# Performance work log

Measured on AMD Instinct MI355X. Metric: run time of the kernel, lower is better.

## Reference

```python
import jax, jax.numpy as jnp
import numpy as np

N_ATOMS = 100000
N_RES = 12500
N_EDGES = 800000
D = 115
D_IN = 37
N_LAYERS = 4


def _sage_conv(x, src, dst, Wl_i, Wr_i, bl_i):
    """PyG SAGEConv (aggr='mean', root_weight=True): lin_l(mean_j x_j) + lin_r(x)."""
    n = x.shape[0]
    deg = jax.ops.segment_sum(jnp.ones(src.shape[0], x.dtype), dst, num_segments=n)
    agg = jax.ops.segment_sum(x[src], dst, num_segments=n)  # [N, D] gather+scatter
    agg = agg / jnp.maximum(deg, 1.0)[:, None]
    return agg @ Wl_i.T + bl_i + x @ Wr_i.T


def setup_inputs() -> dict:
    key = jax.random.key(0)
    ks = jax.random.split(key, 8)
    resid_embedding = jax.random.normal(ks[0], (N_RES, D), dtype=jnp.float32)
    atom_onehot_embedding = jax.random.normal(ks[1], (N_ATOMS, D_IN), dtype=jnp.float32)
    edge_index_atom = jax.random.randint(ks[2], (2, N_EDGES), 0, N_ATOMS, dtype=jnp.int32)
    res2atom_map = jnp.sort(jax.random.randint(ks[3], (N_ATOMS,), 0, N_RES, dtype=jnp.int32))
    ln_W = jax.random.normal(ks[4], (D, D_IN), dtype=jnp.float32) / np.sqrt(D_IN)
    ln_b = jnp.zeros((D,), dtype=jnp.float32)
    Wl = jax.random.normal(ks[5], (N_LAYERS, D, D), dtype=jnp.float32) / np.sqrt(D)
    Wr = jax.random.normal(ks[6], (N_LAYERS, D, D), dtype=jnp.float32) / np.sqrt(D)
    bl = jnp.zeros((N_LAYERS, D), dtype=jnp.float32)
    return {
        "resid_embedding": resid_embedding,
        "atom_onehot_embedding": atom_onehot_embedding,
        "edge_index_atom": edge_index_atom,
        "res2atom_map": res2atom_map,
        "ln_W": ln_W,
        "ln_b": ln_b,
        "Wl": Wl,
        "Wr": Wr,
        "bl": bl,
    }


def reference(resid_embedding, atom_onehot_embedding, edge_index_atom, res2atom_map,
              ln_W, ln_b, Wl, Wr, bl):
    src, dst = edge_index_atom[0], edge_index_atom[1]
    # input projection: Linear(37 -> 115)
    x = atom_onehot_embedding @ ln_W.T + ln_b
    # four chained SAGEConv layers (no activation between them, per source)
    for i in range(N_LAYERS):
        x = _sage_conv(x, src, dst, Wl[i], Wr[i], bl[i])
    # atom2residue: scatter-sum pooling of atom features into residues
    n_res = resid_embedding.shape[0]
    feats_atom = jax.ops.segment_sum(x, res2atom_map, num_segments=n_res)  # [N_RES, D]
    return feats_atom
```

## Files before the change

kernel.cpp:

```cpp
#include <hip/hip_runtime.h>
#include <hip/hip_bf16.h>

#define N_ATOMS 100000
#define N_RES   12500
#define N_EDGES 800000
#define D_IN    37
#define D       115
#define DP      128
#define MPAD    100096
#define N_LAYERS 4
#define SCE     1024
#define NSCB    ((N_ATOMS + SCE - 1) / SCE)
#define KPROJ   64
#define LSTRIDE 72

typedef __bf16 bf16x8 __attribute__((ext_vector_type(8)));
typedef float  f32x4  __attribute__((ext_vector_type(4)));
typedef unsigned int u32x4 __attribute__((ext_vector_type(4)));

__device__ __forceinline__ unsigned short f2bf(float f) {
  unsigned u = __builtin_bit_cast(unsigned, f);
  u += 0x7fffu + ((u >> 16) & 1u);
  return (unsigned short)(u >> 16);
}
__device__ __forceinline__ float bf2f(unsigned short h) {
  unsigned u = ((unsigned)h) << 16;
  return __builtin_bit_cast(float, u);
}
__device__ __forceinline__ bf16x8 ld_frag(const unsigned short* p) {
  u32x4 u = *reinterpret_cast<const u32x4*>(p);
  return __builtin_bit_cast(bf16x8, u);
}

__global__ void k_hist_edges(const int* __restrict__ eidx, int* __restrict__ hist) {
  int e = blockIdx.x * blockDim.x + threadIdx.x;
  if (e < N_EDGES) atomicAdd(&hist[eidx[N_EDGES + e]], 1);
}

__global__ __launch_bounds__(256) void k_scan_part(
    const int* __restrict__ cnt, int* __restrict__ bsum)
{
  __shared__ int sh[256];
  const int t = threadIdx.x, b = blockIdx.x;
  const int base = b * SCE + t * 4;
  int s = 0;
  #pragma unroll
  for (int i = 0; i < 4; ++i) { int id = base + i; if (id < N_ATOMS) s += cnt[id]; }
  sh[t] = s; __syncthreads();
  for (int d = 128; d > 0; d >>= 1) { if (t < d) sh[t] += sh[t + d]; __syncthreads(); }
  if (t == 0) bsum[b] = sh[0];
}
__global__ __launch_bounds__(256) void k_scan_bsum(
    int* __restrict__ bsum, int* __restrict__ total)
{
  __shared__ int sh[256];
  const int t = threadIdx.x;
  int v = (t < NSCB) ? bsum[t] : 0;
  sh[t] = v; __syncthreads();
  for (int d = 1; d < 256; d <<= 1) {
    int u = (t >= d) ? sh[t - d] : 0;
    __syncthreads();
    sh[t] += u;
    __syncthreads();
  }
  if (t < NSCB) bsum[t] = sh[t] - v;
  if (t == 255) *total = sh[255];
}
__global__ __launch_bounds__(256) void k_scan_final(
    const int* __restrict__ cnt, const int* __restrict__ bsum,
    int* __restrict__ offs, int* __restrict__ cursor, float* __restrict__ invdeg)
{
  __shared__ int sh[256];
  const int t = threadIdx.x, b = blockIdx.x;
  const int base = b * SCE + t * 4;
  int c[4]; int s = 0;
  #pragma unroll
  for (int i = 0; i < 4; ++i) {
    int id = base + i;
    c[i] = (id < N_ATOMS) ? cnt[id] : 0;
    s += c[i];
  }
  sh[t] = s; __syncthreads();
  for (int d = 1; d < 256; d <<= 1) {
    int u = (t >= d) ? sh[t - d] : 0;
    __syncthreads();
    sh[t] += u;
    __syncthreads();
  }
  int run = bsum[b] + sh[t] - s;
  #pragma unroll
  for (int i = 0; i < 4; ++i) {
    int id = base + i;
    if (id < N_ATOMS) {
      offs[id] = run;
      cursor[id] = run;
      invdeg[id] = 1.0f / (float)max(c[i], 1);
      run += c[i];
    }
  }
}

__global__ __launch_bounds__(256) void k_res_bounds(
    const int* __restrict__ r2a, int* __restrict__ res_start)
{
  int r = blockIdx.x * blockDim.x + threadIdx.x;
  if (r > N_RES) return;
  int lo = 0, hi = N_ATOMS;
  while (lo < hi) {
    int mid = (lo + hi) >> 1;
    if (r2a[mid] < r) lo = mid + 1; else hi = mid;
  }
  res_start[r] = lo;
}

__global__ void k_fill(const int* __restrict__ eidx, int* __restrict__ cursor,
                       int* __restrict__ srcs) {
  int e = blockIdx.x * blockDim.x + threadIdx.x;
  if (e < N_EDGES) {
    int s = eidx[e], d = eidx[N_EDGES + e];
    int pos = atomicAdd(&cursor[d], 1);
    srcs[pos] = s;
  }
}

__global__ void k_convw(const float* __restrict__ Wl, const float* __restrict__ Wr,
                        unsigned short* __restrict__ wpad)
{
  const int k = threadIdx.x;
  const int c = blockIdx.x;
  const int m = blockIdx.y;
  const float* src = (m < 4) ? (Wl + m * D * D) : (Wr + (m - 4) * D * D);
  unsigned short v = 0;
  if (c < D && k < D) v = f2bf(src[c * D + k]);
  wpad[(m * 128 + c) * 128 + k] = v;
}

__global__ __launch_bounds__(256) void k_proj(
    const float* __restrict__ A, const float* __restrict__ Wf,
    const float* __restrict__ bf, unsigned short* __restrict__ xout)
{
  __shared__ unsigned short sA[128 * LSTRIDE];
  __shared__ unsigned short sW[128 * LSTRIDE];
  const int t = threadIdx.x;
  const int r0 = blockIdx.x * 128;

  for (int idx = t; idx < 128 * KPROJ; idx += 256) {
    const int row = idx >> 6, k = idx & 63;
    const int gr = r0 + row;
    unsigned short v = 0;
    if (k < D_IN && gr < N_ATOMS) v = f2bf(A[(size_t)gr * D_IN + k]);
    sA[row * LSTRIDE + k] = v;
  }
  for (int idx = t; idx < 128 * KPROJ; idx += 256) {
    const int col = idx >> 6, k = idx & 63;
    unsigned short v = 0;
    if (col < D && k < D_IN) v = f2bf(Wf[col * D_IN + k]);
    sW[col * LSTRIDE + k] = v;
  }
  __syncthreads();

  const int lane = t & 63;
  const int wid  = t >> 6;
  const int wrow = wid * 32;
  const int lrow = lane & 15;
  const int koff = (lane >> 4) * 8;

  f32x4 acc[2][8];
  #pragma unroll
  for (int i = 0; i < 2; ++i)
    #pragma unroll
    for (int j = 0; j < 8; ++j)
      acc[i][j] = (f32x4){0.f, 0.f, 0.f, 0.f};

  #pragma unroll
  for (int ks = 0; ks < 2; ++ks) {
    const int k0 = ks * 32 + koff;
    bf16x8 a0 = ld_frag(&sA[(wrow + lrow) * LSTRIDE + k0]);
    bf16x8 a1 = ld_frag(&sA[(wrow + 16 + lrow) * LSTRIDE + k0]);
    #pragma unroll
    for (int ct = 0; ct < 8; ++ct) {
      bf16x8 b = ld_frag(&sW[(ct * 16 + lrow) * LSTRIDE + k0]);
      acc[0][ct] = __builtin_amdgcn_mfma_f32_16x16x32_bf16(a0, b, acc[0][ct], 0, 0, 0);
      acc[1][ct] = __builtin_amdgcn_mfma_f32_16x16x32_bf16(a1, b, acc[1][ct], 0, 0, 0);
    }
  }

  const int ocol = lane & 15;
  const int orow = (lane >> 4) * 4;
  #pragma unroll
  for (int ct = 0; ct < 8; ++ct) {
    const int col = ct * 16 + ocol;
    const float bv = (col < D) ? bf[col] : 0.f;
    #pragma unroll
    for (int rt = 0; rt < 2; ++rt) {
      #pragma unroll
      for (int j = 0; j < 4; ++j) {
        const int grow = r0 + wrow + rt * 16 + orow + j;
        if (grow < N_ATOMS)
          xout[(size_t)grow * DP + col] = f2bf(acc[rt][ct][j] + bv);
      }
    }
  }
}

__global__ __launch_bounds__(256) void k_agg(
    const unsigned int* __restrict__ xin, const int* __restrict__ row_start,
    const int* __restrict__ srcs, const float* __restrict__ invdeg,
    unsigned int* __restrict__ aggout)
{
  const int w = (int)((blockIdx.x * 256 + threadIdx.x) >> 6);
  const int lane = threadIdx.x & 63;
  if (w >= N_ATOMS) return;
  const int beg = row_start[w], end = row_start[w + 1];
  float a0 = 0.f, a1 = 0.f;
  for (int base = beg; base < end; base += 16) {
    const int m = end - base;
    int sidx = 0;
    if (lane < 16 && lane < m) sidx = srcs[base + lane];
    #pragma unroll
    for (int j = 0; j < 16; ++j) {
      const int s = __shfl(sidx, j);
      const unsigned int v = xin[(size_t)s * 64 + lane];
      if (j < m) {
        a0 += bf2f((unsigned short)(v & 0xffffu));
        a1 += bf2f((unsigned short)(v >> 16));
      }
    }
  }
  const float sc = invdeg[w];
  unsigned int o = (unsigned int)f2bf(a0 * sc) | ((unsigned int)f2bf(a1 * sc) << 16);
  aggout[w * 64 + lane] = o;
}

__global__ __launch_bounds__(256) void k_gemm(
    const unsigned short* __restrict__ agg,
    const unsigned short* __restrict__ xin,
    const unsigned short* __restrict__ wl,
    const unsigned short* __restrict__ wr,
    const float* __restrict__ bias,
    unsigned short* __restrict__ xout)
{
  const int lane = threadIdx.x & 63;
  const int wid  = threadIdx.x >> 6;
  const int row0 = blockIdx.x * 128 + wid * 32;
  const int lrow = lane & 15;
  const int koff = (lane >> 4) * 8;

  f32x4 acc[2][8];
  #pragma unroll
  for (int i = 0; i < 2; ++i)
    #pragma unroll
    for (int j = 0; j < 8; ++j)
      acc[i][j] = (f32x4){0.f, 0.f, 0.f, 0.f};

  #pragma unroll
  for (int s = 0; s < 2; ++s) {
    const unsigned short* X = s ? xin : agg;
    const unsigned short* W = s ? wr : wl;
    #pragma unroll
    for (int ks = 0; ks < 4; ++ks) {
      const int k0 = ks * 32 + koff;
      bf16x8 a0 = ld_frag(&X[(size_t)(row0 + lrow) * DP + k0]);
      bf16x8 a1 = ld_frag(&X[(size_t)(row0 + 16 + lrow) * DP + k0]);
      #pragma unroll
      for (int ct = 0; ct < 8; ++ct) {
        bf16x8 b = ld_frag(&W[(ct * 16 + lrow) * DP + k0]);
        acc[0][ct] = __builtin_amdgcn_mfma_f32_16x16x32_bf16(a0, b, acc[0][ct], 0, 0, 0);
        acc[1][ct] = __builtin_amdgcn_mfma_f32_16x16x32_bf16(a1, b, acc[1][ct], 0, 0, 0);
      }
    }
  }

  const int ocol = lane & 15;
  const int orow = (lane >> 4) * 4;
  #pragma unroll
  for (int ct = 0; ct < 8; ++ct) {
    const int col = ct * 16 + ocol;
    const float bv = (col < D) ? bias[col] : 0.f;
    #pragma unroll
    for (int rt = 0; rt < 2; ++rt) {
      #pragma unroll
      for (int j = 0; j < 4; ++j) {
        const int grow = row0 + rt * 16 + orow + j;
        if (grow < N_ATOMS)
          xout[(size_t)grow * DP + col] = f2bf(acc[rt][ct][j] + bv);
      }
    }
  }
}

__global__ __launch_bounds__(256) void k_pool(
    const unsigned int* __restrict__ x, const int* __restrict__ res_start,
    float* __restrict__ out)
{
  const int r = (int)((blockIdx.x * 256 + threadIdx.x) >> 6);
  const int lane = threadIdx.x & 63;
  if (r >= N_RES) return;
  const int beg = res_start[r], end = res_start[r + 1];
  float a0 = 0.f, a1 = 0.f;
  for (int a = beg; a < end; ++a) {
    unsigned int v = x[a * 64 + lane];
    a0 += bf2f((unsigned short)(v & 0xffffu));
    a1 += bf2f((unsigned short)(v >> 16));
  }
  const int c0 = lane * 2;
  if (c0 < D)     out[(size_t)r * D + c0]     = a0;
  if (c0 + 1 < D) out[(size_t)r * D + c0 + 1] = a1;
}

extern "C" void kernel_launch(void* const* d_in, const int* in_sizes, int n_in,
                              void* d_out, int out_size, void* d_ws, size_t ws_size,
                              hipStream_t stream)
{
  (void)in_sizes; (void)n_in; (void)out_size; (void)ws_size;
  const float* atom_emb = (const float*)d_in[1];
  const int*   eidx     = (const int*)d_in[2];
  const int*   r2a      = (const int*)d_in[3];
  const float* lnW      = (const float*)d_in[4];
  const float* lnb      = (const float*)d_in[5];
  const float* Wl       = (const float*)d_in[6];
  const float* Wr       = (const float*)d_in[7];
  const float* bl       = (const float*)d_in[8];
  float* out = (float*)d_out;

  char* p = (char*)d_ws;
  auto alloc = [&](size_t b) { char* r = p; p += (b + 255) & ~(size_t)255; return r; };
  unsigned short* xb0  = (unsigned short*)alloc((size_t)MPAD * DP * 2);
  unsigned short* xb1  = (unsigned short*)alloc((size_t)MPAD * DP * 2);
  unsigned short* xb2  = (unsigned short*)alloc((size_t)MPAD * DP * 2);
  unsigned short* wpad = (unsigned short*)alloc((size_t)8 * 128 * 128 * 2);
  int*   hist      = (int*)alloc((size_t)N_ATOMS * 4);
  int*   row_start = (int*)alloc((size_t)(N_ATOMS + 1) * 4);
  int*   cursor    = (int*)alloc((size_t)N_ATOMS * 4);
  float* invdeg    = (float*)alloc((size_t)N_ATOMS * 4);
  int*   srcs      = (int*)alloc((size_t)N_EDGES * 4);
  int*   bsum      = (int*)alloc((size_t)256 * 4);
  int*   res_start = (int*)alloc((size_t)(N_RES + 1) * 4);

  hipMemsetAsync(hist, 0, (size_t)N_ATOMS * 4, stream);

  k_convw<<<dim3(128, 8), 128, 0, stream>>>(Wl, Wr, wpad);
  k_hist_edges<<<(N_EDGES + 255) / 256, 256, 0, stream>>>(eidx, hist);
  k_scan_part<<<NSCB, 256, 0, stream>>>(hist, bsum);
  k_scan_bsum<<<1, 256, 0, stream>>>(bsum, row_start + N_ATOMS);
  k_scan_final<<<NSCB, 256, 0, stream>>>(hist, bsum, row_start, cursor, invdeg);
  k_res_bounds<<<(N_RES + 1 + 255) / 256, 256, 0, stream>>>(r2a, res_start);
  k_fill<<<(N_EDGES + 255) / 256, 256, 0, stream>>>(eidx, cursor, srcs);
  k_proj<<<MPAD / 128, 256, 0, stream>>>(atom_emb, lnW, lnb, xb0);

  unsigned short* bufs[3] = {xb0, xb1, xb2};
  int cur = 0;
  for (int l = 0; l < N_LAYERS; ++l) {
    unsigned short* xin  = bufs[cur];
    unsigned short* aggb = bufs[(cur + 1) % 3];
    unsigned short* xo   = bufs[(cur + 2) % 3];
    k_agg<<<(N_ATOMS * 64) / 256, 256, 0, stream>>>(
        (const unsigned int*)xin, row_start, srcs, invdeg, (unsigned int*)aggb);
    k_gemm<<<MPAD / 128, 256, 0, stream>>>(
        aggb, xin, wpad + (size_t)l * 16384, wpad + (size_t)(4 + l) * 16384,
        bl + (size_t)l * D, xo);
    cur = (cur + 2) % 3;
  }
  k_pool<<<(N_RES * 64) / 256, 256, 0, stream>>>(
      (const unsigned int*)bufs[cur], res_start, out);
}
```

Before: 732.6 us.

## Fuse neighbor mean aggregation into per-layer GEMM via LDS tile

Merges the separate aggregation and GEMM kernels into one per-layer kernel. Each 128-row block first gathers neighbor features, with 16 threads per row each loading 16-byte chunks, and writes the scaled mean into a padded LDS tile. It then runs the MFMA GEMM from LDS for the aggregated term and from global memory for the root term. This removes the global write and re-read of the aggregated buffer and one launch per layer. The cost is less parallelism in the gather (one block per 128 rows, 782 blocks), sequential per-row loops within each thread group, and higher LDS usage that may reduce occupancy.

```diff
diff --git a/kernel.cpp b/kernel.cpp
--- a/kernel.cpp
+++ b/kernel.cpp
@@ -13,6 +13,7 @@
 #define NSCB    ((N_ATOMS + SCE - 1) / SCE)
 #define KPROJ   64
 #define LSTRIDE 72
+#define LSTR2   136
 
 typedef __bf16 bf16x8 __attribute__((ext_vector_type(8)));
 typedef float  f32x4  __attribute__((ext_vector_type(4)));
@@ -203,46 +204,59 @@
   }
 }
 
-__global__ __launch_bounds__(256) void k_agg(
-    const unsigned int* __restrict__ xin, const int* __restrict__ row_start,
-    const int* __restrict__ srcs, const float* __restrict__ invdeg,
-    unsigned int* __restrict__ aggout)
-{
-  const int w = (int)((blockIdx.x * 256 + threadIdx.x) >> 6);
-  const int lane = threadIdx.x & 63;
-  if (w >= N_ATOMS) return;
-  const int beg = row_start[w], end = row_start[w + 1];
-  float a0 = 0.f, a1 = 0.f;
-  for (int base = beg; base < end; base += 16) {
-    const int m = end - base;
-    int sidx = 0;
-    if (lane < 16 && lane < m) sidx = srcs[base + lane];
-    #pragma unroll
-    for (int j = 0; j < 16; ++j) {
-      const int s = __shfl(sidx, j);
-      const unsigned int v = xin[(size_t)s * 64 + lane];
-      if (j < m) {
-        a0 += bf2f((unsigned short)(v & 0xffffu));
-        a1 += bf2f((unsigned short)(v >> 16));
-      }
-    }
-  }
-  const float sc = invdeg[w];
-  unsigned int o = (unsigned int)f2bf(a0 * sc) | ((unsigned int)f2bf(a1 * sc) << 16);
-  aggout[w * 64 + lane] = o;
-}
-
-__global__ __launch_bounds__(256) void k_gemm(
-    const unsigned short* __restrict__ agg,
+__global__ __launch_bounds__(256) void k_layer(
     const unsigned short* __restrict__ xin,
+    const int* __restrict__ row_start,
+    const int* __restrict__ srcs,
+    const float* __restrict__ invdeg,
     const unsigned short* __restrict__ wl,
     const unsigned short* __restrict__ wr,
     const float* __restrict__ bias,
     unsigned short* __restrict__ xout)
 {
-  const int lane = threadIdx.x & 63;
-  const int wid  = threadIdx.x >> 6;
-  const int row0 = blockIdx.x * 128 + wid * 32;
+  __shared__ unsigned short sAgg[128 * LSTR2];
+  const int t = threadIdx.x;
+  const int r0 = blockIdx.x * 128;
+  const int rp = t >> 4;
+  const int ql = t & 15;
+
+  for (int i = 0; i < 8; ++i) {
+    const int row = rp * 8 + i;
+    const int grow = r0 + row;
+    float a[8] = {0.f,0.f,0.f,0.f,0.f,0.f,0.f,0.f};
+    float sc = 0.f;
+    if (grow < N_ATOMS) {
+      const int beg = row_start[grow], end = row_start[grow + 1];
+      sc = invdeg[grow];
+      for (int b2 = beg; b2 < end; b2 += 16) {
+        const int m = end - b2;
+        int sidx = 0;
+        if (ql < m) sidx = srcs[b2 + ql];
+        #pragma unroll
+        for (int j = 0; j < 16; ++j) {
+          if (j < m) {
+            const int s = __shfl(sidx, (t & 48) + j);
+            const u32x4 v = *(reinterpret_cast<const u32x4*>(xin + (size_t)s * DP) + ql);
+            #pragma unroll
+            for (int q = 0; q < 4; ++q) {
+              a[2*q]   += bf2f((unsigned short)(v[q] & 0xffffu));
+              a[2*q+1] += bf2f((unsigned short)(v[q] >> 16));
+            }
+          }
+        }
+      }
+    }
+    unsigned int w[4];
+    #pragma unroll
+    for (int q = 0; q < 4; ++q)
+      w[q] = (unsigned int)f2bf(a[2*q] * sc) | ((unsigned int)f2bf(a[2*q+1] * sc) << 16);
+    *reinterpret_cast<u32x4*>(&sAgg[row * LSTR2 + ql * 8]) = (u32x4){w[0], w[1], w[2], w[3]};
+  }
+  __syncthreads();
+
+  const int lane = t & 63;
+  const int wid  = t >> 6;
+  const int wrow = wid * 32;
   const int lrow = lane & 15;
   const int koff = (lane >> 4) * 8;
 
@@ -254,20 +268,27 @@
       acc[i][j] = (f32x4){0.f, 0.f, 0.f, 0.f};
 
   #pragma unroll
-  for (int s = 0; s < 2; ++s) {
-    const unsigned short* X = s ? xin : agg;
-    const unsigned short* W = s ? wr : wl;
-    #pragma unroll
-    for (int ks = 0; ks < 4; ++ks) {
-      const int k0 = ks * 32 + koff;
-      bf16x8 a0 = ld_frag(&X[(size_t)(row0 + lrow) * DP + k0]);
-      bf16x8 a1 = ld_frag(&X[(size_t)(row0 + 16 + lrow) * DP + k0]);
-      #pragma unroll
-      for (int ct = 0; ct < 8; ++ct) {
-        bf16x8 b = ld_frag(&W[(ct * 16 + lrow) * DP + k0]);
-        acc[0][ct] = __builtin_amdgcn_mfma_f32_16x16x32_bf16(a0, b, acc[0][ct], 0, 0, 0);
-        acc[1][ct] = __builtin_amdgcn_mfma_f32_16x16x32_bf16(a1, b, acc[1][ct], 0, 0, 0);
-      }
+  for (int ks = 0; ks < 4; ++ks) {
+    const int k0 = ks * 32 + koff;
+    bf16x8 a0 = ld_frag(&sAgg[(wrow + lrow) * LSTR2 + k0]);
+    bf16x8 a1 = ld_frag(&sAgg[(wrow + 16 + lrow) * LSTR2 + k0]);
+    #pragma unroll
+    for (int ct = 0; ct < 8; ++ct) {
+      bf16x8 b = ld_frag(&wl[(ct * 16 + lrow) * DP + k0]);
+      acc[0][ct] = __builtin_amdgcn_mfma_f32_16x16x32_bf16(a0, b, acc[0][ct], 0, 0, 0);
+      acc[1][ct] = __builtin_amdgcn_mfma_f32_16x16x32_bf16(a1, b, acc[1][ct], 0, 0, 0);
+    }
+  }
+  #pragma unroll
+  for (int ks = 0; ks < 4; ++ks) {
+    const int k0 = ks * 32 + koff;
+    bf16x8 a0 = ld_frag(&xin[(size_t)(r0 + wrow + lrow) * DP + k0]);
+    bf16x8 a1 = ld_frag(&xin[(size_t)(r0 + wrow + 16 + lrow) * DP + k0]);
+    #pragma unroll
+    for (int ct = 0; ct < 8; ++ct) {
+      bf16x8 b = ld_frag(&wr[(ct * 16 + lrow) * DP + k0]);
+      acc[0][ct] = __builtin_amdgcn_mfma_f32_16x16x32_bf16(a0, b, acc[0][ct], 0, 0, 0);
+      acc[1][ct] = __builtin_amdgcn_mfma_f32_16x16x32_bf16(a1, b, acc[1][ct], 0, 0, 0);
     }
   }
 
@@ -281,7 +302,7 @@
     for (int rt = 0; rt < 2; ++rt) {
       #pragma unroll
       for (int j = 0; j < 4; ++j) {
-        const int grow = row0 + rt * 16 + orow + j;
+        const int grow = r0 + wrow + rt * 16 + orow + j;
         if (grow < N_ATOMS)
           xout[(size_t)grow * DP + col] = f2bf(acc[rt][ct][j] + bv);
       }
@@ -327,7 +348,6 @@
   auto alloc = [&](size_t b) { char* r = p; p += (b + 255) & ~(size_t)255; return r; };
   unsigned short* xb0  = (unsigned short*)alloc((size_t)MPAD * DP * 2);
   unsigned short* xb1  = (unsigned short*)alloc((size_t)MPAD * DP * 2);
-  unsigned short* xb2  = (unsigned short*)alloc((size_t)MPAD * DP * 2);
   unsigned short* wpad = (unsigned short*)alloc((size_t)8 * 128 * 128 * 2);
   int*   hist      = (int*)alloc((size_t)N_ATOMS * 4);
   int*   row_start = (int*)alloc((size_t)(N_ATOMS + 1) * 4);
@@ -348,19 +368,15 @@
   k_fill<<<(N_EDGES + 255) / 256, 256, 0, stream>>>(eidx, cursor, srcs);
   k_proj<<<MPAD / 128, 256, 0, stream>>>(atom_emb, lnW, lnb, xb0);
 
-  unsigned short* bufs[3] = {xb0, xb1, xb2};
-  int cur = 0;
+  unsigned short* cur = xb0;
+  unsigned short* nxt = xb1;
   for (int l = 0; l < N_LAYERS; ++l) {
-    unsigned short* xin  = bufs[cur];
-    unsigned short* aggb = bufs[(cur + 1) % 3];
-    unsigned short* xo   = bufs[(cur + 2) % 3];
-    k_agg<<<(N_ATOMS * 64) / 256, 256, 0, stream>>>(
-        (const unsigned int*)xin, row_start, srcs, invdeg, (unsigned int*)aggb);
-    k_gemm<<<MPAD / 128, 256, 0, stream>>>(
-        aggb, xin, wpad + (size_t)l * 16384, wpad + (size_t)(4 + l) * 16384,
-        bl + (size_t)l * D, xo);
-    cur = (cur + 2) % 3;
+    k_layer<<<MPAD / 128, 256, 0, stream>>>(
+        cur, row_start, srcs, invdeg,
+        wpad + (size_t)l * 16384, wpad + (size_t)(4 + l) * 16384,
+        bl + (size_t)l * D, nxt);
+    unsigned short* tmp = cur; cur = nxt; nxt = tmp;
   }
   k_pool<<<(N_RES * 64) / 256, 256, 0, stream>>>(
-      (const unsigned int*)bufs[cur], res_start, out);
-}
+      (const unsigned int*)cur, res_start, out);
+}
```

After: 788.5 us. 7.6% more time.

## Exploit layer linearity: propagate raw features, pool per hop, fold weights

Applied to the files above, without the earlier changes.

There is no activation between the SAGE layers, so the whole network is linear. The per-layer MFMA GEMMs are replaced by repeated mean-aggregation of the projected features. Each hop's result is pooled into residues, and a small weight-polynomial matrix per hop is built from Wl, Wr and the biases, with a ones column carrying the bias. A final fp32 kernel combines the five pooled stacks with these matrices. This removes four full-size atom GEMMs and their global traffic. In exchange it adds extra pooling passes, tiny serial matrix-product launches and a scalar, non-MFMA final contraction, and it changes where rounding happens.

```diff
diff --git a/kernel.cpp b/kernel.cpp
--- a/kernel.cpp
+++ b/kernel.cpp
@@ -123,16 +123,60 @@
   }
 }
 
-__global__ void k_convw(const float* __restrict__ Wl, const float* __restrict__ Wr,
-                        unsigned short* __restrict__ wpad)
-{
-  const int k = threadIdx.x;
-  const int c = blockIdx.x;
-  const int m = blockIdx.y;
-  const float* src = (m < 4) ? (Wl + m * D * D) : (Wr + (m - 4) * D * D);
-  unsigned short v = 0;
-  if (c < D && k < D) v = f2bf(src[c * D + k]);
-  wpad[(m * 128 + c) * 128 + k] = v;
+__global__ void k_buildR(const float* __restrict__ Wl, const float* __restrict__ Wr,
+                         const float* __restrict__ bl, float* __restrict__ R)
+{
+  int idx = blockIdx.x * 256 + threadIdx.x;
+  if (idx >= 4 * 2 * 128 * 128) return;
+  int c = idx & 127, k = (idx >> 7) & 127, side = (idx >> 14) & 1, l = idx >> 15;
+  float v = 0.f;
+  if (side == 0) {
+    if (k < D && c < D) v = Wl[(size_t)l * D * D + c * D + k];
+  } else {
+    if (k < D && c < D) v = Wr[(size_t)l * D * D + c * D + k];
+    else if (k == D && c < D) v = bl[l * D + c];
+    else if (k == D && c == D) v = 1.f;
+  }
+  R[idx] = v;
+}
+
+__global__ void k_ginit(float* __restrict__ G) {
+  int idx = blockIdx.x * 256 + threadIdx.x;
+  if (idx < 16384) G[idx] = ((idx >> 7) == (idx & 127)) ? 1.f : 0.f;
+}
+
+__global__ __launch_bounds__(256) void k_mdp(
+    const float* __restrict__ Gp, float* __restrict__ Gn,
+    const float* __restrict__ Rl, const float* __restrict__ Rr, int lmax)
+{
+  const int b = blockIdx.x;
+  const int k = b >> 2;
+  const int r = (b & 3) * 32 + (threadIdx.x >> 3);
+  const int c0 = (threadIdx.x & 7) * 16;
+  float acc[16];
+  #pragma unroll
+  for (int q = 0; q < 16; ++q) acc[q] = 0.f;
+  if (k <= lmax - 1) {
+    const float* g = Gp + (size_t)k * 16384 + r * 128;
+    for (int j = 0; j < 128; ++j) {
+      const float a = g[j];
+      const float* rr = Rr + j * 128 + c0;
+      #pragma unroll
+      for (int q = 0; q < 16; ++q) acc[q] += a * rr[q];
+    }
+  }
+  if (k >= 1) {
+    const float* g = Gp + (size_t)(k - 1) * 16384 + r * 128;
+    for (int j = 0; j < 128; ++j) {
+      const float a = g[j];
+      const float* rl = Rl + j * 128 + c0;
+      #pragma unroll
+      for (int q = 0; q < 16; ++q) acc[q] += a * rl[q];
+    }
+  }
+  float* o = Gn + (size_t)k * 16384 + r * 128 + c0;
+  #pragma unroll
+  for (int q = 0; q < 16; ++q) o[q] = acc[q];
 }
 
 __global__ __launch_bounds__(256) void k_proj(
@@ -196,8 +240,11 @@
       #pragma unroll
       for (int j = 0; j < 4; ++j) {
         const int grow = r0 + wrow + rt * 16 + orow + j;
-        if (grow < N_ATOMS)
-          xout[(size_t)grow * DP + col] = f2bf(acc[rt][ct][j] + bv);
+        if (grow < N_ATOMS) {
+          unsigned short ov = (col == D) ? (unsigned short)0x3F80
+                                         : f2bf(acc[rt][ct][j] + bv);
+          xout[(size_t)grow * DP + col] = ov;
+        }
       }
     }
   }
@@ -232,66 +279,9 @@
   aggout[w * 64 + lane] = o;
 }
 
-__global__ __launch_bounds__(256) void k_gemm(
-    const unsigned short* __restrict__ agg,
-    const unsigned short* __restrict__ xin,
-    const unsigned short* __restrict__ wl,
-    const unsigned short* __restrict__ wr,
-    const float* __restrict__ bias,
-    unsigned short* __restrict__ xout)
-{
-  const int lane = threadIdx.x & 63;
-  const int wid  = threadIdx.x >> 6;
-  const int row0 = blockIdx.x * 128 + wid * 32;
-  const int lrow = lane & 15;
-  const int koff = (lane >> 4) * 8;
-
-  f32x4 acc[2][8];
-  #pragma unroll
-  for (int i = 0; i < 2; ++i)
-    #pragma unroll
-    for (int j = 0; j < 8; ++j)
-      acc[i][j] = (f32x4){0.f, 0.f, 0.f, 0.f};
-
-  #pragma unroll
-  for (int s = 0; s < 2; ++s) {
-    const unsigned short* X = s ? xin : agg;
-    const unsigned short* W = s ? wr : wl;
-    #pragma unroll
-    for (int ks = 0; ks < 4; ++ks) {
-      const int k0 = ks * 32 + koff;
-      bf16x8 a0 = ld_frag(&X[(size_t)(row0 + lrow) * DP + k0]);
-      bf16x8 a1 = ld_frag(&X[(size_t)(row0 + 16 + lrow) * DP + k0]);
-      #pragma unroll
-      for (int ct = 0; ct < 8; ++ct) {
-        bf16x8 b = ld_frag(&W[(ct * 16 + lrow) * DP + k0]);
-        acc[0][ct] = __builtin_amdgcn_mfma_f32_16x16x32_bf16(a0, b, acc[0][ct], 0, 0, 0);
-        acc[1][ct] = __builtin_amdgcn_mfma_f32_16x16x32_bf16(a1, b, acc[1][ct], 0, 0, 0);
-      }
-    }
-  }
-
-  const int ocol = lane & 15;
-  const int orow = (lane >> 4) * 4;
-  #pragma unroll
-  for (int ct = 0; ct < 8; ++ct) {
-    const int col = ct * 16 + ocol;
-    const float bv = (col < D) ? bias[col] : 0.f;
-    #pragma unroll
-    for (int rt = 0; rt < 2; ++rt) {
-      #pragma unroll
-      for (int j = 0; j < 4; ++j) {
-        const int grow = row0 + rt * 16 + orow + j;
-        if (grow < N_ATOMS)
-          xout[(size_t)grow * DP + col] = f2bf(acc[rt][ct][j] + bv);
-      }
-    }
-  }
-}
-
-__global__ __launch_bounds__(256) void k_pool(
+__global__ __launch_bounds__(256) void k_pool128(
     const unsigned int* __restrict__ x, const int* __restrict__ res_start,
-    float* __restrict__ out)
+    float* __restrict__ outp)
 {
   const int r = (int)((blockIdx.x * 256 + threadIdx.x) >> 6);
   const int lane = threadIdx.x & 63;
@@ -299,13 +289,29 @@
   const int beg = res_start[r], end = res_start[r + 1];
   float a0 = 0.f, a1 = 0.f;
   for (int a = beg; a < end; ++a) {
-    unsigned int v = x[a * 64 + lane];
+    unsigned int v = x[(size_t)a * 64 + lane];
     a0 += bf2f((unsigned short)(v & 0xffffu));
     a1 += bf2f((unsigned short)(v >> 16));
   }
-  const int c0 = lane * 2;
-  if (c0 < D)     out[(size_t)r * D + c0]     = a0;
-  if (c0 + 1 < D) out[(size_t)r * D + c0 + 1] = a1;
+  outp[(size_t)r * 128 + lane * 2]     = a0;
+  outp[(size_t)r * 128 + lane * 2 + 1] = a1;
+}
+
+__global__ __launch_bounds__(256) void k_final(
+    const float* __restrict__ pstack, const float* __restrict__ G,
+    float* __restrict__ out)
+{
+  const int r = blockIdx.x * 2 + (threadIdx.x >> 7);
+  const int c = threadIdx.x & 127;
+  if (r >= N_RES) return;
+  float acc = 0.f;
+  #pragma unroll
+  for (int k = 0; k < 5; ++k) {
+    const float* pr = pstack + ((size_t)k * N_RES + r) * 128;
+    const float* g  = G + (size_t)k * 16384;
+    for (int j = 0; j < 128; ++j) acc += pr[j] * g[j * 128 + c];
+  }
+  if (c < D) out[(size_t)r * D + c] = acc;
 }
 
 extern "C" void kernel_launch(void* const* d_in, const int* in_sizes, int n_in,
@@ -325,10 +331,12 @@
 
   char* p = (char*)d_ws;
   auto alloc = [&](size_t b) { char* r = p; p += (b + 255) & ~(size_t)255; return r; };
-  unsigned short* xb0  = (unsigned short*)alloc((size_t)MPAD * DP * 2);
-  unsigned short* xb1  = (unsigned short*)alloc((size_t)MPAD * DP * 2);
-  unsigned short* xb2  = (unsigned short*)alloc((size_t)MPAD * DP * 2);
-  unsigned short* wpad = (unsigned short*)alloc((size_t)8 * 128 * 128 * 2);
+  unsigned short* y0   = (unsigned short*)alloc((size_t)MPAD * DP * 2);
+  unsigned short* y1   = (unsigned short*)alloc((size_t)MPAD * DP * 2);
+  float* pstack = (float*)alloc((size_t)5 * N_RES * 128 * 4);
+  float* R      = (float*)alloc((size_t)4 * 2 * 16384 * 4);
+  float* Ga     = (float*)alloc((size_t)5 * 16384 * 4);
+  float* Gb     = (float*)alloc((size_t)5 * 16384 * 4);
   int*   hist      = (int*)alloc((size_t)N_ATOMS * 4);
   int*   row_start = (int*)alloc((size_t)(N_ATOMS + 1) * 4);
   int*   cursor    = (int*)alloc((size_t)N_ATOMS * 4);
@@ -339,28 +347,34 @@
 
   hipMemsetAsync(hist, 0, (size_t)N_ATOMS * 4, stream);
 
-  k_convw<<<dim3(128, 8), 128, 0, stream>>>(Wl, Wr, wpad);
   k_hist_edges<<<(N_EDGES + 255) / 256, 256, 0, stream>>>(eidx, hist);
   k_scan_part<<<NSCB, 256, 0, stream>>>(hist, bsum);
   k_scan_bsum<<<1, 256, 0, stream>>>(bsum, row_start + N_ATOMS);
   k_scan_final<<<NSCB, 256, 0, stream>>>(hist, bsum, row_start, cursor, invdeg);
   k_res_bounds<<<(N_RES + 1 + 255) / 256, 256, 0, stream>>>(r2a, res_start);
   k_fill<<<(N_EDGES + 255) / 256, 256, 0, stream>>>(eidx, cursor, srcs);
-  k_proj<<<MPAD / 128, 256, 0, stream>>>(atom_emb, lnW, lnb, xb0);
-
-  unsigned short* bufs[3] = {xb0, xb1, xb2};
-  int cur = 0;
-  for (int l = 0; l < N_LAYERS; ++l) {
-    unsigned short* xin  = bufs[cur];
-    unsigned short* aggb = bufs[(cur + 1) % 3];
-    unsigned short* xo   = bufs[(cur + 2) % 3];
+
+  k_buildR<<<512, 256, 0, stream>>>(Wl, Wr, bl, R);
+  k_ginit<<<64, 256, 0, stream>>>(Ga);
+  float* gc = Ga; float* gn = Gb;
+  for (int l = 1; l <= N_LAYERS; ++l) {
+    k_mdp<<<(l + 1) * 4, 256, 0, stream>>>(
+        gc, gn, R + (size_t)(l - 1) * 2 * 16384, R + ((size_t)(l - 1) * 2 + 1) * 16384, l);
+    float* tmp = gc; gc = gn; gn = tmp;
+  }
+
+  k_proj<<<MPAD / 128, 256, 0, stream>>>(atom_emb, lnW, lnb, y0);
+  k_pool128<<<(N_RES * 64) / 256, 256, 0, stream>>>(
+      (const unsigned int*)y0, res_start, pstack);
+  unsigned short* cur = y0;
+  unsigned short* nxt = y1;
+  for (int k = 1; k <= N_LAYERS; ++k) {
     k_agg<<<(N_ATOMS * 64) / 256, 256, 0, stream>>>(
-        (const unsigned int*)xin, row_start, srcs, invdeg, (unsigned int*)aggb);
-    k_gemm<<<MPAD / 128, 256, 0, stream>>>(
-        aggb, xin, wpad + (size_t)l * 16384, wpad + (size_t)(4 + l) * 16384,
-        bl + (size_t)l * D, xo);
-    cur = (cur + 2) % 3;
-  }
-  k_pool<<<(N_RES * 64) / 256, 256, 0, stream>>>(
-      (const unsigned int*)bufs[cur], res_start, out);
-}
+        (const unsigned int*)cur, row_start, srcs, invdeg, (unsigned int*)nxt);
+    k_pool128<<<(N_RES * 64) / 256, 256, 0, stream>>>(
+        (const unsigned int*)nxt, res_start, pstack + (size_t)k * N_RES * 128);
+    unsigned short* tmp = cur; cur = nxt; nxt = tmp;
+  }
+
+  k_final<<<(N_RES + 1) / 2, 256, 0, stream>>>(pstack, gc, out);
+}
```

Result: slower. 991.1 us (+35.3%).
